# Kernel optimization log

Measured on AMD Instinct MI355X. Metric: run time of the kernel, lower is better.

The kernel has to match this reference:

```python
import jax, jax.numpy as jnp
import numpy as np
from jax import lax

B, CIN, COUT, K, H, W, HE = 16, 64, 64, 3, 128, 128, 8
PAD = 1

def setup_inputs() -> dict:
    key = jax.random.key(0)
    ks = jax.random.split(key, 11)
    r = lambda k, s: jax.random.normal(k, s, dtype=jnp.float32)
    return {
        'x': r(ks[0], (B, CIN, H, W)),
        'h': r(ks[1], (B, HE)),
        'fc_w': r(ks[2], (16 * K * K, HE)) * 0.1,
        'fc_b': r(ks[3], (16 * K * K,)) * 0.1,
        'w1': r(ks[4], (32, 16)) * 0.1,
        'b1': r(ks[5], (32,)) * 0.1,
        'w2': r(ks[6], (32, 32)) * 0.1,
        'b2': r(ks[7], (32,)) * 0.1,
        'w3': r(ks[8], (COUT * CIN, 32)) * 0.05,
        'b3': r(ks[9], (COUT * CIN,)) * 0.05,
        'bias': r(ks[10], (COUT,)) * 0.05,
    }

def _kernel_net(h, fc_w, fc_b, w1, b1, w2, b2, w3, b3):
    lrelu = lambda v: jax.nn.leaky_relu(v, 0.01)
    k = lrelu(h @ fc_w.T + fc_b)                       # [B, 16*K*K]
    k = k.reshape(B, 16, K, K)                          # [B, 16, K, K]
    k = lrelu(jnp.einsum('oc,bckl->bokl', w1, k) + b1[:, None, None])
    k = lrelu(jnp.einsum('oc,bckl->bokl', w2, k) + b2[:, None, None])
    k = jnp.einsum('oc,bckl->bokl', w3, k) + b3[:, None, None]  # [B, COUT*CIN, K, K]
    return k

def reference(x, h, fc_w, fc_b, w1, b1, w2, b2, w3, b3, bias):
    kernels = _kernel_net(h, fc_w, fc_b, w1, b1, w2, b2, w3, b3)
    # per-sample conv as a single grouped conv: batch folded into groups
    weight = kernels.reshape(B * COUT, CIN, K, K)       # [B*COUT, CIN, K, K]
    xg = x.reshape(1, B * CIN, H, W)
    y = lax.conv_general_dilated(
        xg, weight,
        window_strides=(1, 1), padding=[(PAD, PAD), (PAD, PAD)],
        dimension_numbers=('NCHW', 'OIHW', 'NCHW'),
        feature_group_count=B)
    y = y.reshape(B, COUT, H, W) + bias[None, :, None, None]
    return y
```

## Files before the change

### kernel.cpp

```cpp
#include <hip/hip_runtime.h>

#define BB   16
#define CINC 64
#define COUTC 64
#define HH   128
#define WW   128

typedef _Float16 f16x8 __attribute__((ext_vector_type(8)));
typedef float f32x4 __attribute__((ext_vector_type(4)));

__device__ __forceinline__ float lrelu(float v) {
    return fmaxf(v, 0.f) + 0.01f * fminf(v, 0.f);
}

__global__ void hyper_k2_kernel(const float* __restrict__ h,
                                const float* __restrict__ fc_w,
                                const float* __restrict__ fc_b,
                                const float* __restrict__ w1,
                                const float* __restrict__ b1,
                                const float* __restrict__ w2,
                                const float* __restrict__ b2,
                                float* __restrict__ k2_out) {
    int b = blockIdx.x;
    int t = threadIdx.x;
    __shared__ float hs[8];
    __shared__ float k0s[144];
    __shared__ float k1s[288];
    if (t < 8) hs[t] = h[b * 8 + t];
    __syncthreads();
    if (t < 144) {
        float acc = fc_b[t];
        #pragma unroll
        for (int c = 0; c < 8; ++c) acc += hs[c] * fc_w[t * 8 + c];
        k0s[t] = lrelu(acc);
    }
    __syncthreads();
    for (int idx = t; idx < 288; idx += 256) {
        int o = idx / 9, tap = idx % 9;
        float acc = b1[o];
        #pragma unroll
        for (int c = 0; c < 16; ++c) acc += w1[o * 16 + c] * k0s[c * 9 + tap];
        k1s[idx] = lrelu(acc);
    }
    __syncthreads();
    for (int idx = t; idx < 288; idx += 256) {
        int o = idx / 9, tap = idx % 9;
        float acc = b2[o];
        #pragma unroll
        for (int c = 0; c < 32; ++c) acc += w2[o * 32 + c] * k1s[c * 9 + tap];
        k2_out[b * 288 + idx] = lrelu(acc);
    }
}

__global__ void hyper_wfrag_kernel(const float* __restrict__ k2,
                                   const float* __restrict__ w3,
                                   const float* __restrict__ b3,
                                   _Float16* __restrict__ wf) {
    int co = blockIdx.x;
    int b  = blockIdx.y;
    int ci = threadIdx.x;
    __shared__ float k2s[288];
    for (int i = ci; i < 288; i += 64) k2s[i] = k2[b * 288 + i];
    __syncthreads();
    int o = co * CINC + ci;
    float wrow[32];
    #pragma unroll
    for (int c = 0; c < 32; ++c) wrow[c] = w3[o * 32 + c];
    float bb = b3[o];
    int chunk = ci >> 5;
    int g     = (ci >> 3) & 3;
    int j     = ci & 7;
    int lane  = (g << 4) | (co & 15);
    int coT   = co >> 4;
    #pragma unroll
    for (int tap = 0; tap < 9; ++tap) {
        float acc = bb;
        #pragma unroll
        for (int c = 0; c < 32; ++c) acc += wrow[c] * k2s[c * 9 + tap];
        size_t frag = ((size_t)(b * 9 + tap) * 2 + chunk) * 4 + coT;
        wf[frag * 512 + lane * 8 + j] = (_Float16)acc;
    }
}

__global__ __launch_bounds__(128)
void conv_mfma_kernel(const float* __restrict__ x,
                      const _Float16* __restrict__ wf,
                      const float* __restrict__ bias,
                      float* __restrict__ out) {
    __shared__ __align__(16) char xs[324 * 128];

    const int b   = blockIdx.z;
    const int x0  = blockIdx.x * 16;
    const int y0  = blockIdx.y * 16;
    const int tid = threadIdx.x;
    const int lane = tid & 63;
    const int w    = tid >> 6;
    const int lc   = lane & 15;
    const int g    = lane >> 4;

    f32x4 acc[8][4];
    #pragma unroll
    for (int m = 0; m < 8; ++m)
        #pragma unroll
        for (int n = 0; n < 4; ++n)
            acc[m][n] = (f32x4){0.f, 0.f, 0.f, 0.f};

    const float* xb = x + (size_t)b * CINC * HH * WW;
    const f16x8* wfb = (const f16x8*)wf;

    for (int chunk = 0; chunk < 2; ++chunk) {
        if (chunk) __syncthreads();
        for (int idx = tid; idx < 16 * 324; idx += 128) {
            int cp   = idx / 324;
            int p    = idx - cp * 324;
            int srow = p / 18;
            int scol = p - srow * 18;
            int gy = y0 - 1 + srow;
            int gx = x0 - 1 + scol;
            int ci = chunk * 32 + cp * 2;
            float v0 = 0.f, v1 = 0.f;
            if (gy >= 0 && gy < HH && gx >= 0 && gx < WW) {
                const float* px = xb + (size_t)ci * (HH * WW) + gy * WW + gx;
                v0 = px[0];
                v1 = px[HH * WW];
            }
            _Float16 h0 = (_Float16)v0, h1 = (_Float16)v1;
            _Float16 l0 = (_Float16)(v0 - (float)h0);
            _Float16 l1 = (_Float16)(v1 - (float)h1);
            unsigned hp = (unsigned)__builtin_bit_cast(unsigned short, h0) |
                          ((unsigned)__builtin_bit_cast(unsigned short, h1) << 16);
            unsigned lp = (unsigned)__builtin_bit_cast(unsigned short, l0) |
                          ((unsigned)__builtin_bit_cast(unsigned short, l1) << 16);
            char* base = xs + p * 128 + (cp & 3) * 4;
            int gsl = cp >> 2;
            *(unsigned*)(base + (((gsl)     + p) & 7) * 16) = hp;
            *(unsigned*)(base + (((4 + gsl) + p) & 7) * 16) = lp;
        }
        __syncthreads();

        f16x8 B0[4], B1[4];
        {
            size_t fb = ((size_t)(b * 9 + 0) * 2 + chunk) * 4;
            #pragma unroll
            for (int n = 0; n < 4; ++n) B0[n] = wfb[(fb + n) * 64 + lane];
        }

        #pragma unroll 1
        for (int tap = 0; tap < 9; ++tap) {
            if (tap < 8) {
                size_t fb = ((size_t)(b * 9 + tap + 1) * 2 + chunk) * 4;
                #pragma unroll
                for (int n = 0; n < 4; ++n) B1[n] = wfb[(fb + n) * 64 + lane];
            }
            int ky = tap / 3;
            int kx = tap - ky * 3;
            int scol = lc + kx;
            #pragma unroll
            for (int m = 0; m < 8; ++m) {
                int srow = w * 8 + m + ky;
                int p = srow * 18 + scol;
                const char* pb = xs + p * 128;
                f16x8 Ah = *(const f16x8*)(pb + (((g)     + p) & 7) * 16);
                f16x8 Al = *(const f16x8*)(pb + (((4 + g) + p) & 7) * 16);
                #pragma unroll
                for (int n = 0; n < 4; ++n) {
                    acc[m][n] = __builtin_amdgcn_mfma_f32_16x16x32_f16(Ah, B0[n], acc[m][n], 0, 0, 0);
                    acc[m][n] = __builtin_amdgcn_mfma_f32_16x16x32_f16(Al, B0[n], acc[m][n], 0, 0, 0);
                }
            }
            if (tap < 8) {
                #pragma unroll
                for (int n = 0; n < 4; ++n) B0[n] = B1[n];
            }
        }
    }

    float bval[4];
    #pragma unroll
    for (int n = 0; n < 4; ++n) bval[n] = bias[n * 16 + lc];
    #pragma unroll
    for (int m = 0; m < 8; ++m) {
        int y  = y0 + w * 8 + m;
        int xx = x0 + g * 4;
        #pragma unroll
        for (int n = 0; n < 4; ++n) {
            int co = n * 16 + lc;
            f32x4 r = acc[m][n];
            r += bval[n];
            *(f32x4*)(out + (((size_t)(b * COUTC + co) * HH + y) * WW + xx)) = r;
        }
    }
}

extern "C" void kernel_launch(void* const* d_in, const int* in_sizes, int n_in,
                              void* d_out, int out_size, void* d_ws, size_t ws_size,
                              hipStream_t stream) {
    const float* x    = (const float*)d_in[0];
    const float* h    = (const float*)d_in[1];
    const float* fc_w = (const float*)d_in[2];
    const float* fc_b = (const float*)d_in[3];
    const float* w1   = (const float*)d_in[4];
    const float* b1   = (const float*)d_in[5];
    const float* w2   = (const float*)d_in[6];
    const float* b2   = (const float*)d_in[7];
    const float* w3   = (const float*)d_in[8];
    const float* b3   = (const float*)d_in[9];
    const float* bias = (const float*)d_in[10];
    float* out = (float*)d_out;

    float* k2 = (float*)d_ws;
    _Float16* wfrag = (_Float16*)((char*)d_ws + 18432);

    hyper_k2_kernel<<<dim3(BB), dim3(256), 0, stream>>>(h, fc_w, fc_b, w1, b1, w2, b2, k2);
    hyper_wfrag_kernel<<<dim3(COUTC, BB), dim3(64), 0, stream>>>(k2, w3, b3, wfrag);
    conv_mfma_kernel<<<dim3(WW / 16, HH / 16, BB), dim3(128), 0, stream>>>(x, wfrag, bias, out);
}
```

Baseline: 234.8 us.

## Pre-split input into fp16 hi/lo channel-last layout and fuse hypernet kernels

Adds a pre-pass that converts x into a channel-last buffer of fp16 high/low split pairs, so the conv kernel can fill shared memory with plain 16-byte copies. Halo pixels read from a zero page instead of taking a branchy conversion path. The hypernetwork's two kernels are merged into one that recomputes the small MLP in every block, and the conv moves to 256 threads with a smaller per-wave tile. The cost is an extra 64MB write and read of the transformed input, plus a dependence on workspace size, with the old path kept as fallback.

```diff
diff --git a/kernel.cpp b/kernel.cpp
--- a/kernel.cpp
+++ b/kernel.cpp
@@ -7,6 +7,7 @@
 #define WW   128
 
 typedef _Float16 f16x8 __attribute__((ext_vector_type(8)));
+typedef _Float16 f16x4 __attribute__((ext_vector_type(4)));
 typedef float f32x4 __attribute__((ext_vector_type(4)));
 
 __device__ __forceinline__ float lrelu(float v) {
@@ -88,7 +89,6 @@
                       const float* __restrict__ bias,
                       float* __restrict__ out) {
     __shared__ __align__(16) char xs[324 * 128];
-
     const int b   = blockIdx.z;
     const int x0  = blockIdx.x * 16;
     const int y0  = blockIdx.y * 16;
@@ -144,7 +144,6 @@
             #pragma unroll
             for (int n = 0; n < 4; ++n) B0[n] = wfb[(fb + n) * 64 + lane];
         }
-
         #pragma unroll 1
         for (int tap = 0; tap < 9; ++tap) {
             if (tap < 8) {
@@ -192,6 +191,223 @@
     }
 }
 
+__global__ void hyper_fused_kernel(const float* __restrict__ h,
+                                   const float* __restrict__ fc_w,
+                                   const float* __restrict__ fc_b,
+                                   const float* __restrict__ w1,
+                                   const float* __restrict__ b1,
+                                   const float* __restrict__ w2,
+                                   const float* __restrict__ b2,
+                                   const float* __restrict__ w3,
+                                   const float* __restrict__ b3,
+                                   _Float16* __restrict__ wf,
+                                   float* __restrict__ zp) {
+    int co = blockIdx.x;
+    int b  = blockIdx.y;
+    int t  = threadIdx.x;
+    __shared__ float hs[8];
+    __shared__ float k0s[144];
+    __shared__ float k1s[288];
+    __shared__ float k2s[288];
+    if (t < 8) hs[t] = h[b * 8 + t];
+    if (co == 0 && b == 0) ((f32x4*)zp)[t] = (f32x4){0.f, 0.f, 0.f, 0.f};
+    __syncthreads();
+    for (int i = t; i < 144; i += 64) {
+        float a = fc_b[i];
+        #pragma unroll
+        for (int c = 0; c < 8; ++c) a += hs[c] * fc_w[i * 8 + c];
+        k0s[i] = lrelu(a);
+    }
+    __syncthreads();
+    for (int i = t; i < 288; i += 64) {
+        int o = i / 9, tap = i % 9;
+        float a = b1[o];
+        #pragma unroll
+        for (int c = 0; c < 16; ++c) a += w1[o * 16 + c] * k0s[c * 9 + tap];
+        k1s[i] = lrelu(a);
+    }
+    __syncthreads();
+    for (int i = t; i < 288; i += 64) {
+        int o = i / 9, tap = i % 9;
+        float a = b2[o];
+        #pragma unroll
+        for (int c = 0; c < 32; ++c) a += w2[o * 32 + c] * k1s[c * 9 + tap];
+        k2s[i] = lrelu(a);
+    }
+    __syncthreads();
+    int ci = t;
+    int o = co * CINC + ci;
+    float wrow[32];
+    #pragma unroll
+    for (int c = 0; c < 32; ++c) wrow[c] = w3[o * 32 + c];
+    float bb = b3[o];
+    int chunk = ci >> 5;
+    int g     = (ci >> 3) & 3;
+    int j     = ci & 7;
+    int lane  = (g << 4) | (co & 15);
+    #pragma unroll
+    for (int tap = 0; tap < 9; ++tap) {
+        float acc = bb;
+        #pragma unroll
+        for (int c = 0; c < 32; ++c) acc += wrow[c] * k2s[c * 9 + tap];
+        size_t frag = ((size_t)(b * 9 + tap) * 2 + chunk) * 4 + (co >> 4);
+        wf[frag * 512 + lane * 8 + j] = (_Float16)acc;
+    }
+}
+
+__global__ __launch_bounds__(256)
+void xsplit_kernel(const float* __restrict__ x, _Float16* __restrict__ xt) {
+    __shared__ __align__(16) char lt[64 * 256];
+    const int xh = blockIdx.x;
+    const int y  = blockIdx.y;
+    const int b  = blockIdx.z;
+    const int t  = threadIdx.x;
+    const int cig = t >> 4;
+    const int pxq = t & 15;
+    const int chunk = cig >> 3;
+    const int g     = (cig >> 1) & 3;
+    const int jh    = cig & 1;
+    const int ci0   = chunk * 32 + g * 8 + jh * 4;
+    const int x0    = xh * 64;
+
+    f32x4 xv[4];
+    #pragma unroll
+    for (int r = 0; r < 4; ++r)
+        xv[r] = *(const f32x4*)(x + (((size_t)(b * CINC + ci0 + r) * HH + y) * WW + x0 + pxq * 4));
+
+    const int off_hi = (chunk << 7) + (g << 4) + (jh << 3);
+    #pragma unroll
+    for (int ii = 0; ii < 4; ++ii) {
+        int px = pxq * 4 + ii;
+        f16x4 hv, lv;
+        #pragma unroll
+        for (int r = 0; r < 4; ++r) {
+            float v = xv[r][ii];
+            _Float16 hh = (_Float16)v;
+            hv[r] = hh;
+            lv[r] = (_Float16)(v - (float)hh);
+        }
+        int sw = (px & 7) << 4;
+        *(f16x4*)(lt + (px << 8) + ((off_hi)      ^ sw)) = hv;
+        *(f16x4*)(lt + (px << 8) + ((off_hi + 64) ^ sw)) = lv;
+    }
+    __syncthreads();
+
+    char* dst = (char*)xt + (((size_t)(b * HH + y) * WW + x0) << 8);
+    #pragma unroll
+    for (int r = 0; r < 4; ++r) {
+        int lu = r * 256 + t;
+        int px = lu >> 4;
+        int sl = lu & 15;
+        f16x8 v = *(const f16x8*)(lt + (px << 8) + ((sl ^ (px & 7)) << 4));
+        *(f16x8*)(dst + (size_t)lu * 16) = v;
+    }
+}
+
+__global__ __launch_bounds__(256)
+void conv_mfma2_kernel(const _Float16* __restrict__ xt,
+                       const _Float16* __restrict__ wf,
+                       const float* __restrict__ bias,
+                       const float* __restrict__ zp,
+                       float* __restrict__ out) {
+    __shared__ __align__(16) char xs[324 * 64];
+
+    const int b   = blockIdx.z;
+    const int x0  = blockIdx.x * 16;
+    const int y0  = blockIdx.y * 16;
+    const int tid = threadIdx.x;
+    const int lane = tid & 63;
+    const int w    = tid >> 6;
+    const int lc   = lane & 15;
+    const int g    = lane >> 4;
+
+    f32x4 acc[4][4];
+    #pragma unroll
+    for (int m = 0; m < 4; ++m)
+        #pragma unroll
+        for (int n = 0; n < 4; ++n)
+            acc[m][n] = (f32x4){0.f, 0.f, 0.f, 0.f};
+
+    const char* xtb = (const char*)xt;
+    const char* zpb = (const char*)zp;
+    const f16x8* wfb = (const f16x8*)wf;
+
+    for (int vc = 0; vc < 4; ++vc) {
+        const int chunk = vc >> 1;
+        const int plane = vc & 1;
+        if (vc) __syncthreads();
+        #pragma unroll
+        for (int i = 0; i < 5; ++i) {
+            int u = ((i * 4 + w) << 6) + lane;
+            int p = u >> 2, s = u & 3;
+            int srow = p / 18;
+            int scol = p - srow * 18;
+            int gy = y0 - 1 + srow;
+            int gx = x0 - 1 + scol;
+            const char* gp;
+            if ((unsigned)gy < HH && (unsigned)gx < WW)
+                gp = xtb + ((((size_t)b * HH + gy) * WW + gx) << 8)
+                         + (chunk << 7) + (plane << 6) + (((s - p) & 3) << 4);
+            else
+                gp = zpb + ((u & 63) << 4);
+            f16x8 v = *(const f16x8*)gp;
+            *(f16x8*)(xs + (u << 4)) = v;
+        }
+        if (tid < 16) {
+            int u = 1280 + tid;
+            int p = u >> 2, s = u & 3;
+            int srow = p / 18;
+            int scol = p - srow * 18;
+            int gy = y0 - 1 + srow;
+            int gx = x0 - 1 + scol;
+            const char* gp;
+            if ((unsigned)gy < HH && (unsigned)gx < WW)
+                gp = xtb + ((((size_t)b * HH + gy) * WW + gx) << 8)
+                         + (chunk << 7) + (plane << 6) + (((s - p) & 3) << 4);
+            else
+                gp = zpb + ((u & 63) << 4);
+            f16x8 v = *(const f16x8*)gp;
+            *(f16x8*)(xs + (u << 4)) = v;
+        }
+        __syncthreads();
+
+        #pragma unroll 1
+        for (int tap = 0; tap < 9; ++tap) {
+            size_t fb = ((size_t)(b * 9 + tap) * 2 + chunk) * 4;
+            f16x8 B[4];
+            #pragma unroll
+            for (int n = 0; n < 4; ++n) B[n] = wfb[(fb + n) * 64 + lane];
+            int ky = tap / 3;
+            int kx = tap - ky * 3;
+            #pragma unroll
+            for (int m = 0; m < 4; ++m) {
+                int srow = (w << 2) + m + ky;
+                int p = srow * 18 + lc + kx;
+                f16x8 A = *(const f16x8*)(xs + (p << 6) + (((g + p) & 3) << 4));
+                #pragma unroll
+                for (int n = 0; n < 4; ++n)
+                    acc[m][n] = __builtin_amdgcn_mfma_f32_16x16x32_f16(A, B[n], acc[m][n], 0, 0, 0);
+            }
+        }
+    }
+
+    float bval[4];
+    #pragma unroll
+    for (int n = 0; n < 4; ++n) bval[n] = bias[n * 16 + lc];
+    #pragma unroll
+    for (int m = 0; m < 4; ++m) {
+        int y  = y0 + (w << 2) + m;
+        int xx = x0 + g * 4;
+        #pragma unroll
+        for (int n = 0; n < 4; ++n) {
+            int co = n * 16 + lc;
+            f32x4 r = acc[m][n];
+            r += bval[n];
+            *(f32x4*)(out + (((size_t)(b * COUTC + co) * HH + y) * WW + xx)) = r;
+        }
+    }
+}
+
 extern "C" void kernel_launch(void* const* d_in, const int* in_sizes, int n_in,
                               void* d_out, int out_size, void* d_ws, size_t ws_size,
                               hipStream_t stream) {
@@ -208,10 +424,25 @@
     const float* bias = (const float*)d_in[10];
     float* out = (float*)d_out;
 
-    float* k2 = (float*)d_ws;
-    _Float16* wfrag = (_Float16*)((char*)d_ws + 18432);
-
-    hyper_k2_kernel<<<dim3(BB), dim3(256), 0, stream>>>(h, fc_w, fc_b, w1, b1, w2, b2, k2);
-    hyper_wfrag_kernel<<<dim3(COUTC, BB), dim3(64), 0, stream>>>(k2, w3, b3, wfrag);
-    conv_mfma_kernel<<<dim3(WW / 16, HH / 16, BB), dim3(128), 0, stream>>>(x, wfrag, bias, out);
-}
+    const size_t ZP_BYTES = 1024;
+    const size_t WF_BYTES = (size_t)BB * 9 * 2 * 4 * 512 * sizeof(_Float16);
+    const size_t XT_BYTES = (size_t)BB * HH * WW * 256;
+    const size_t NEED = ZP_BYTES + WF_BYTES + XT_BYTES;
+
+    if (ws_size >= NEED) {
+        float*     zp = (float*)d_ws;
+        _Float16*  wf = (_Float16*)((char*)d_ws + ZP_BYTES);
+        _Float16*  xt = (_Float16*)((char*)d_ws + ZP_BYTES + WF_BYTES);
+        hyper_fused_kernel<<<dim3(COUTC, BB), dim3(64), 0, stream>>>(
+            h, fc_w, fc_b, w1, b1, w2, b2, w3, b3, wf, zp);
+        xsplit_kernel<<<dim3(2, HH, BB), dim3(256), 0, stream>>>(x, xt);
+        conv_mfma2_kernel<<<dim3(WW / 16, HH / 16, BB), dim3(256), 0, stream>>>(
+            xt, wf, bias, zp, out);
+    } else {
+        float* k2 = (float*)d_ws;
+        _Float16* wfrag = (_Float16*)((char*)d_ws + 18432);
+        hyper_k2_kernel<<<dim3(BB), dim3(256), 0, stream>>>(h, fc_w, fc_b, w1, b1, w2, b2, k2);
+        hyper_wfrag_kernel<<<dim3(COUTC, BB), dim3(64), 0, stream>>>(k2, w3, b3, wfrag);
+        conv_mfma_kernel<<<dim3(WW / 16, HH / 16, BB), dim3(128), 0, stream>>>(x, wfrag, bias, out);
+    }
+}
```

Result: faster. 195.1 us (-16.9%).

## Pre-split input to fp16 hi/lo layout and double-buffer conv via direct LDS loads

Applied to the files above, without the earlier changes.

A new prep kernel converts x once into a pixel-major fp16 hi/lo interleaved buffer in workspace, and in the same launch computes the hypernetwork weight fragments and a zero-pad block, merging three launches into two. The conv kernel now uses 256 threads and stages tiles with global_load_lds into double-buffered LDS, so the next channel plane loads while MFMAs run on the current one. The cost being targeted is the per-tile fp32-to-fp16 split and the unoverlapped staging done in every conv block. In exchange it adds a full extra write and read of the transformed input (about twice the fp16 size of x) through global memory.

```diff
diff --git a/kernel.cpp b/kernel.cpp
--- a/kernel.cpp
+++ b/kernel.cpp
@@ -7,87 +7,152 @@
 #define WW   128
 
 typedef _Float16 f16x8 __attribute__((ext_vector_type(8)));
+typedef _Float16 f16x4 __attribute__((ext_vector_type(4)));
 typedef float f32x4 __attribute__((ext_vector_type(4)));
+
+typedef const __attribute__((address_space(1))) void* gas_ptr;
+typedef __attribute__((address_space(3))) void* las_ptr;
 
 __device__ __forceinline__ float lrelu(float v) {
     return fmaxf(v, 0.f) + 0.01f * fminf(v, 0.f);
 }
 
-__global__ void hyper_k2_kernel(const float* __restrict__ h,
-                                const float* __restrict__ fc_w,
-                                const float* __restrict__ fc_b,
-                                const float* __restrict__ w1,
-                                const float* __restrict__ b1,
-                                const float* __restrict__ w2,
-                                const float* __restrict__ b2,
-                                float* __restrict__ k2_out) {
-    int b = blockIdx.x;
-    int t = threadIdx.x;
-    __shared__ float hs[8];
-    __shared__ float k0s[144];
-    __shared__ float k1s[288];
-    if (t < 8) hs[t] = h[b * 8 + t];
-    __syncthreads();
-    if (t < 144) {
-        float acc = fc_b[t];
-        #pragma unroll
-        for (int c = 0; c < 8; ++c) acc += hs[c] * fc_w[t * 8 + c];
-        k0s[t] = lrelu(acc);
+__device__ __forceinline__ void gload_lds16(const void* g, void* l) {
+    __builtin_amdgcn_global_load_lds((gas_ptr)g, (las_ptr)l, 16, 0, 0);
+}
+
+__global__ __launch_bounds__(256)
+void prep_kernel(const float* __restrict__ x,
+                 const float* __restrict__ h,
+                 const float* __restrict__ fc_w,
+                 const float* __restrict__ fc_b,
+                 const float* __restrict__ w1,
+                 const float* __restrict__ b1,
+                 const float* __restrict__ w2,
+                 const float* __restrict__ b2,
+                 const float* __restrict__ w3,
+                 const float* __restrict__ b3,
+                 _Float16* __restrict__ wf,
+                 float* __restrict__ zp,
+                 _Float16* __restrict__ xt) {
+    __shared__ __align__(16) char smem[16384];
+    const int bid = blockIdx.x;
+    const int t   = threadIdx.x;
+
+    if (bid < 4096) {
+        char* lt = smem;
+        const int xh = bid & 1;
+        const int y  = (bid >> 1) & 127;
+        const int b  = bid >> 8;
+        const int cig = t >> 4;
+        const int pxq = t & 15;
+        const int chunk = cig >> 3;
+        const int g     = (cig >> 1) & 3;
+        const int jh    = cig & 1;
+        const int ci0   = chunk * 32 + g * 8 + jh * 4;
+        const int x0    = xh * 64;
+
+        f32x4 xv[4];
+        #pragma unroll
+        for (int r = 0; r < 4; ++r)
+            xv[r] = *(const f32x4*)(x + (((size_t)(b * CINC + ci0 + r) * HH + y) * WW + x0 + pxq * 4));
+
+        const int off_hi = (chunk << 7) + (g << 4) + (jh << 3);
+        #pragma unroll
+        for (int ii = 0; ii < 4; ++ii) {
+            int px = pxq * 4 + ii;
+            f16x4 hv, lv;
+            #pragma unroll
+            for (int r = 0; r < 4; ++r) {
+                float v = xv[r][ii];
+                _Float16 hh = (_Float16)v;
+                hv[r] = hh;
+                lv[r] = (_Float16)(v - (float)hh);
+            }
+            int sw = (px & 7) << 4;
+            *(f16x4*)(lt + (px << 8) + ((off_hi)      ^ sw)) = hv;
+            *(f16x4*)(lt + (px << 8) + ((off_hi + 64) ^ sw)) = lv;
+        }
+        __syncthreads();
+
+        char* dst = (char*)xt + (((size_t)(b * HH + y) * WW + x0) << 8);
+        #pragma unroll
+        for (int r = 0; r < 4; ++r) {
+            int lu = r * 256 + t;
+            int px = lu >> 4;
+            int sl = lu & 15;
+            f16x8 v = *(const f16x8*)(lt + (px << 8) + ((sl ^ (px & 7)) << 4));
+            *(f16x8*)(dst + (size_t)lu * 16) = v;
+        }
+    } else {
+        float* hs  = (float*)smem;
+        float* k0s = hs + 8;
+        float* k1s = k0s + 144;
+        float* k2s = k1s + 288;
+        const int j   = bid - 4096;
+        const int b   = j & 15;
+        const int cog = j >> 4;
+
+        if (t < 8) hs[t] = h[b * 8 + t];
+        if (j == 0 && t < 64) *(f32x4*)((char*)zp + t * 16) = (f32x4){0.f, 0.f, 0.f, 0.f};
+        __syncthreads();
+        if (t < 144) {
+            float a = fc_b[t];
+            #pragma unroll
+            for (int c = 0; c < 8; ++c) a += hs[c] * fc_w[t * 8 + c];
+            k0s[t] = lrelu(a);
+        }
+        __syncthreads();
+        for (int i = t; i < 288; i += 256) {
+            int o = i / 9, tap = i % 9;
+            float a = b1[o];
+            #pragma unroll
+            for (int c = 0; c < 16; ++c) a += w1[o * 16 + c] * k0s[c * 9 + tap];
+            k1s[i] = lrelu(a);
+        }
+        __syncthreads();
+        for (int i = t; i < 288; i += 256) {
+            int o = i / 9, tap = i % 9;
+            float a = b2[o];
+            #pragma unroll
+            for (int c = 0; c < 32; ++c) a += w2[o * 32 + c] * k1s[c * 9 + tap];
+            k2s[i] = lrelu(a);
+        }
+        __syncthreads();
+
+        const int co = cog * 16 + (t >> 4);
+        const int ci_base = (t & 15) * 4;
+        #pragma unroll 1
+        for (int cq = 0; cq < 4; ++cq) {
+            int ci = ci_base + cq;
+            int o = co * CINC + ci;
+            float wrow[32];
+            #pragma unroll
+            for (int c = 0; c < 32; ++c) wrow[c] = w3[o * 32 + c];
+            float bb3 = b3[o];
+            int chunk = ci >> 5;
+            int g     = (ci >> 3) & 3;
+            int jj    = ci & 7;
+            int lane  = (g << 4) | (co & 15);
+            #pragma unroll
+            for (int tap = 0; tap < 9; ++tap) {
+                float a = bb3;
+                #pragma unroll
+                for (int c = 0; c < 32; ++c) a += wrow[c] * k2s[c * 9 + tap];
+                size_t frag = ((size_t)(b * 9 + tap) * 2 + chunk) * 4 + (co >> 4);
+                wf[frag * 512 + lane * 8 + jj] = (_Float16)a;
+            }
+        }
     }
-    __syncthreads();
-    for (int idx = t; idx < 288; idx += 256) {
-        int o = idx / 9, tap = idx % 9;
-        float acc = b1[o];
-        #pragma unroll
-        for (int c = 0; c < 16; ++c) acc += w1[o * 16 + c] * k0s[c * 9 + tap];
-        k1s[idx] = lrelu(acc);
-    }
-    __syncthreads();
-    for (int idx = t; idx < 288; idx += 256) {
-        int o = idx / 9, tap = idx % 9;
-        float acc = b2[o];
-        #pragma unroll
-        for (int c = 0; c < 32; ++c) acc += w2[o * 32 + c] * k1s[c * 9 + tap];
-        k2_out[b * 288 + idx] = lrelu(acc);
-    }
-}
-
-__global__ void hyper_wfrag_kernel(const float* __restrict__ k2,
-                                   const float* __restrict__ w3,
-                                   const float* __restrict__ b3,
-                                   _Float16* __restrict__ wf) {
-    int co = blockIdx.x;
-    int b  = blockIdx.y;
-    int ci = threadIdx.x;
-    __shared__ float k2s[288];
-    for (int i = ci; i < 288; i += 64) k2s[i] = k2[b * 288 + i];
-    __syncthreads();
-    int o = co * CINC + ci;
-    float wrow[32];
-    #pragma unroll
-    for (int c = 0; c < 32; ++c) wrow[c] = w3[o * 32 + c];
-    float bb = b3[o];
-    int chunk = ci >> 5;
-    int g     = (ci >> 3) & 3;
-    int j     = ci & 7;
-    int lane  = (g << 4) | (co & 15);
-    int coT   = co >> 4;
-    #pragma unroll
-    for (int tap = 0; tap < 9; ++tap) {
-        float acc = bb;
-        #pragma unroll
-        for (int c = 0; c < 32; ++c) acc += wrow[c] * k2s[c * 9 + tap];
-        size_t frag = ((size_t)(b * 9 + tap) * 2 + chunk) * 4 + coT;
-        wf[frag * 512 + lane * 8 + j] = (_Float16)acc;
-    }
-}
-
-__global__ __launch_bounds__(128)
-void conv_mfma_kernel(const float* __restrict__ x,
-                      const _Float16* __restrict__ wf,
-                      const float* __restrict__ bias,
-                      float* __restrict__ out) {
-    __shared__ __align__(16) char xs[324 * 128];
+}
+
+__global__ __launch_bounds__(256, 3)
+void conv_mfma3_kernel(const _Float16* __restrict__ xt,
+                       const _Float16* __restrict__ wf,
+                       const float* __restrict__ bias,
+                       const float* __restrict__ zp,
+                       float* __restrict__ out) {
+    __shared__ __align__(16) char xs[2][324 * 64];
 
     const int b   = blockIdx.z;
     const int x0  = blockIdx.x * 16;
@@ -98,89 +163,94 @@
     const int lc   = lane & 15;
     const int g    = lane >> 4;
 
-    f32x4 acc[8][4];
-    #pragma unroll
-    for (int m = 0; m < 8; ++m)
+    f32x4 acc[4][4];
+    #pragma unroll
+    for (int m = 0; m < 4; ++m)
         #pragma unroll
         for (int n = 0; n < 4; ++n)
             acc[m][n] = (f32x4){0.f, 0.f, 0.f, 0.f};
 
-    const float* xb = x + (size_t)b * CINC * HH * WW;
+    const char* xtb = (const char*)xt;
+    const char* zpb = (const char*)zp;
     const f16x8* wfb = (const f16x8*)wf;
 
-    for (int chunk = 0; chunk < 2; ++chunk) {
-        if (chunk) __syncthreads();
-        for (int idx = tid; idx < 16 * 324; idx += 128) {
-            int cp   = idx / 324;
-            int p    = idx - cp * 324;
+    auto stage = [&](char* dbuf, int chunk, int plane) {
+        const int cpo = (chunk << 7) + (plane << 6);
+        #pragma unroll
+        for (int i = 0; i < 5; ++i) {
+            int ub = (i * 4 + w) << 6;
+            int u  = ub + lane;
+            int p = u >> 2, s = u & 3;
             int srow = p / 18;
             int scol = p - srow * 18;
             int gy = y0 - 1 + srow;
             int gx = x0 - 1 + scol;
-            int ci = chunk * 32 + cp * 2;
-            float v0 = 0.f, v1 = 0.f;
-            if (gy >= 0 && gy < HH && gx >= 0 && gx < WW) {
-                const float* px = xb + (size_t)ci * (HH * WW) + gy * WW + gx;
-                v0 = px[0];
-                v1 = px[HH * WW];
-            }
-            _Float16 h0 = (_Float16)v0, h1 = (_Float16)v1;
-            _Float16 l0 = (_Float16)(v0 - (float)h0);
-            _Float16 l1 = (_Float16)(v1 - (float)h1);
-            unsigned hp = (unsigned)__builtin_bit_cast(unsigned short, h0) |
-                          ((unsigned)__builtin_bit_cast(unsigned short, h1) << 16);
-            unsigned lp = (unsigned)__builtin_bit_cast(unsigned short, l0) |
-                          ((unsigned)__builtin_bit_cast(unsigned short, l1) << 16);
-            char* base = xs + p * 128 + (cp & 3) * 4;
-            int gsl = cp >> 2;
-            *(unsigned*)(base + (((gsl)     + p) & 7) * 16) = hp;
-            *(unsigned*)(base + (((4 + gsl) + p) & 7) * 16) = lp;
-        }
-        __syncthreads();
-
-        f16x8 B0[4], B1[4];
-        {
-            size_t fb = ((size_t)(b * 9 + 0) * 2 + chunk) * 4;
-            #pragma unroll
-            for (int n = 0; n < 4; ++n) B0[n] = wfb[(fb + n) * 64 + lane];
-        }
-
+            const char* gp;
+            if ((unsigned)gy < HH && (unsigned)gx < WW)
+                gp = xtb + ((((size_t)b * HH + gy) * WW + gx) << 8) + cpo + (((s - p) & 3) << 4);
+            else
+                gp = zpb + ((u & 63) << 4);
+            gload_lds16(gp, dbuf + (ub << 4));
+        }
+        if (tid < 16) {
+            int u = 1280 + tid;
+            int p = u >> 2, s = u & 3;
+            int srow = p / 18;
+            int scol = p - srow * 18;
+            int gy = y0 - 1 + srow;
+            int gx = x0 - 1 + scol;
+            const char* gp;
+            if ((unsigned)gy < HH && (unsigned)gx < WW)
+                gp = xtb + ((((size_t)b * HH + gy) * WW + gx) << 8) + cpo + (((s - p) & 3) << 4);
+            else
+                gp = zpb + ((u & 63) << 4);
+            gload_lds16(gp, dbuf + 1280 * 16);
+        }
+    };
+
+    auto compute = [&](const char* sbuf, int chunk) {
+        size_t fb0 = ((size_t)(b * 9) * 2 + chunk) * 4;
+        f16x8 Bc[4], Bn[4];
+        #pragma unroll
+        for (int n = 0; n < 4; ++n) Bc[n] = wfb[(fb0 + n) * 64 + lane];
         #pragma unroll 1
         for (int tap = 0; tap < 9; ++tap) {
             if (tap < 8) {
                 size_t fb = ((size_t)(b * 9 + tap + 1) * 2 + chunk) * 4;
                 #pragma unroll
-                for (int n = 0; n < 4; ++n) B1[n] = wfb[(fb + n) * 64 + lane];
+                for (int n = 0; n < 4; ++n) Bn[n] = wfb[(fb + n) * 64 + lane];
             }
             int ky = tap / 3;
             int kx = tap - ky * 3;
-            int scol = lc + kx;
-            #pragma unroll
-            for (int m = 0; m < 8; ++m) {
-                int srow = w * 8 + m + ky;
-                int p = srow * 18 + scol;
-                const char* pb = xs + p * 128;
-                f16x8 Ah = *(const f16x8*)(pb + (((g)     + p) & 7) * 16);
-                f16x8 Al = *(const f16x8*)(pb + (((4 + g) + p) & 7) * 16);
+            #pragma unroll
+            for (int m = 0; m < 4; ++m) {
+                int srow = (w << 2) + m + ky;
+                int p = srow * 18 + lc + kx;
+                f16x8 A = *(const f16x8*)(sbuf + (p << 6) + (((g + p) & 3) << 4));
                 #pragma unroll
-                for (int n = 0; n < 4; ++n) {
-                    acc[m][n] = __builtin_amdgcn_mfma_f32_16x16x32_f16(Ah, B0[n], acc[m][n], 0, 0, 0);
-                    acc[m][n] = __builtin_amdgcn_mfma_f32_16x16x32_f16(Al, B0[n], acc[m][n], 0, 0, 0);
-                }
-            }
-            if (tap < 8) {
-                #pragma unroll
-                for (int n = 0; n < 4; ++n) B0[n] = B1[n];
-            }
-        }
+                for (int n = 0; n < 4; ++n)
+                    acc[m][n] = __builtin_amdgcn_mfma_f32_16x16x32_f16(A, Bc[n], acc[m][n], 0, 0, 0);
+            }
+            #pragma unroll
+            for (int n = 0; n < 4; ++n) Bc[n] = Bn[n];
+        }
+    };
+
+    stage((char*)xs[0], 0, 0);
+    __syncthreads();
+    #pragma unroll
+    for (int vc = 0; vc < 4; ++vc) {
+        if (vc < 3) stage((char*)xs[(vc + 1) & 1], (vc + 1) >> 1, (vc + 1) & 1);
+        compute((const char*)xs[vc & 1], vc >> 1);
+        __syncthreads();
     }
 
     float bval[4];
     #pragma unroll
     for (int n = 0; n < 4; ++n) bval[n] = bias[n * 16 + lc];
     #pragma unroll
-    for (int m = 0; m < 8; ++m) {
-        int y  = y0 + w * 8 + m;
+    for (int m = 0; m < 4; ++m) {
+        int y  = y0 + (w << 2) + m;
         int xx = x0 + g * 4;
         #pragma unroll
         for (int n = 0; n < 4; ++n) {
@@ -208,10 +278,14 @@
     const float* bias = (const float*)d_in[10];
     float* out = (float*)d_out;
 
-    float* k2 = (float*)d_ws;
-    _Float16* wfrag = (_Float16*)((char*)d_ws + 18432);
-
-    hyper_k2_kernel<<<dim3(BB), dim3(256), 0, stream>>>(h, fc_w, fc_b, w1, b1, w2, b2, k2);
-    hyper_wfrag_kernel<<<dim3(COUTC, BB), dim3(64), 0, stream>>>(k2, w3, b3, wfrag);
-    conv_mfma_kernel<<<dim3(WW / 16, HH / 16, BB), dim3(128), 0, stream>>>(x, wfrag, bias, out);
-}
+    const size_t ZP_BYTES = 1024;
+    const size_t WF_BYTES = (size_t)BB * 9 * 2 * 4 * 512 * sizeof(_Float16);
+    float*     zp = (float*)d_ws;
+    _Float16*  wf = (_Float16*)((char*)d_ws + ZP_BYTES);
+    _Float16*  xt = (_Float16*)((char*)d_ws + ZP_BYTES + WF_BYTES);
+
+    prep_kernel<<<dim3(4096 + 64), dim3(256), 0, stream>>>(
+        x, h, fc_w, fc_b, w1, b1, w2, b2, w3, b3, wf, zp, xt);
+    conv_mfma3_kernel<<<dim3(WW / 16, HH / 16, BB), dim3(256), 0, stream>>>(
+        xt, wf, bias, zp, out);
+}
```

Measured after the change: 198.1 us. 1.19x faster.
